# Kernel optimization log

Measured on AMD Instinct MI355X. Metric: run time of the kernel, lower is better.

Reference implementation:

```python
import jax, jax.numpy as jnp
import numpy as np

SEG = 24      # segment_size
NH = 8        # n_heads
THETA = 10000.0


def setup_inputs() -> dict:
    key = jax.random.key(0)
    ks = jax.random.split(key, 6)
    B, T, H, W, D = 8, 96, 32, 32, 64
    in_dim = SEG * D          # 1536
    hid_dim = (SEG // 2) * D  # 768
    n_seg = T // SEG          # 4
    x = jax.random.normal(ks[0], (B, T, H, W, D), dtype=jnp.float32)
    # rotary frequencies: freqs_cis[t, j] = exp(i * t * theta^{-2j/hid_dim})
    inv = 1.0 / (THETA ** (np.arange(0, hid_dim, 2, dtype=np.float32) / hid_dim))
    ang = np.arange(n_seg, dtype=np.float32)[:, None] * inv[None, :]  # (n, hid/2)
    freqs_cos = jnp.asarray(np.cos(ang), dtype=jnp.float32)
    freqs_sin = jnp.asarray(np.sin(ang), dtype=jnp.float32)
    s = 0.02
    Wq = jax.random.normal(ks[1], (in_dim, hid_dim), dtype=jnp.float32) * s
    Wk = jax.random.normal(ks[2], (in_dim, hid_dim), dtype=jnp.float32) * s
    Wv = jax.random.normal(ks[3], (in_dim, hid_dim), dtype=jnp.float32) * s
    Wo = jax.random.normal(ks[4], (hid_dim, in_dim), dtype=jnp.float32) * s
    bo = jnp.zeros((in_dim,), dtype=jnp.float32)
    return {"x": x, "freqs_cos": freqs_cos, "freqs_sin": freqs_sin,
            "Wq": Wq, "Wk": Wk, "Wv": Wv, "Wo": Wo, "bo": bo}


def _rope(q, cos, sin):
    # q: (b, n, hid); pairs (even, odd) rotated by complex multiply
    q2 = q.reshape(*q.shape[:-1], -1, 2)
    qr = q2[..., 0] * cos - q2[..., 1] * sin
    qi = q2[..., 0] * sin + q2[..., 1] * cos
    return jnp.stack([qr, qi], axis=-1).reshape(q.shape)


def reference(x, freqs_cos, freqs_sin, Wq, Wk, Wv, Wo, bo):
    B, T, H, W, D = x.shape
    n = T // SEG
    hid = Wq.shape[1]
    hd = hid // NH
    # (b t h w d) -> ((b h w) n (p d)) ; T divisible by SEG so no padding
    xr = jnp.transpose(x, (0, 2, 3, 1, 4)).reshape(B * H * W, T, D)
    xs = xr.reshape(B * H * W, n, SEG * D)
    q = jnp.einsum('bne,eh->bnh', xs, Wq)
    k = jnp.einsum('bne,eh->bnh', xs, Wk)
    v = jnp.einsum('bne,eh->bnh', xs, Wv)
    cos, sin = freqs_cos[:n][None], freqs_sin[:n][None]  # (1, n, hid/2)
    q = _rope(q, cos, sin)
    k = _rope(k, cos, sin)
    # split heads: b n (h d) -> b h n d
    def heads(t):
        return jnp.transpose(t.reshape(B * H * W, n, NH, hd), (0, 2, 1, 3))
    qh, kh, vh = heads(q), heads(k), heads(v)
    scores = jnp.einsum('bhnd,bhmd->bhnm', qh, kh) / jnp.sqrt(jnp.float32(hd))
    attn = jax.nn.softmax(scores, axis=-1)
    o = jnp.einsum('bhnm,bhmd->bhnd', attn, vh)
    o = jnp.transpose(o, (0, 2, 1, 3)).reshape(B * H * W, n, hid)
    o = jnp.einsum('bnh,he->bne', o, Wo) + bo
    # b n (p d) -> b (n p) d -> (B,T,H,W,D)
    o = o.reshape(B * H * W, T, D)
    o = o.reshape(B, H, W, T, D)
    return jnp.transpose(o, (0, 3, 1, 2, 4))
```

## Files before the change

### kernel.cpp

```cpp
#include <hip/hip_runtime.h>
#include <hip/hip_bf16.h>

using bf16 = __hip_bfloat16;
using short8 = __attribute__((ext_vector_type(8))) short;
using floatx4 = __attribute__((ext_vector_type(4))) float;

#define NSEG 4
#define HID 768
#define INDIM 1536
#define NQKV 2304
#define NHEADS 8
#define HD 96

__device__ inline unsigned short f2b(float v) {
  union { float f; unsigned u; } c; c.f = v;
  unsigned r = c.u + 0x7FFF + ((c.u >> 16) & 1);
  return (unsigned short)(r >> 16);
}

__device__ inline void gload16(const void* g, void* l) {
  __builtin_amdgcn_global_load_lds(
      (const __attribute__((address_space(1))) unsigned int*)g,
      (__attribute__((address_space(3))) unsigned int*)l, 16, 0, 0);
}

#define MEMFENCE asm volatile("" ::: "memory")
#define BARRIER do { MEMFENCE; __builtin_amdgcn_s_barrier(); MEMFENCE; } while (0)

#define PHASE(par, q, LOADB, STAGES, VMW) do {                                 \
    short8 a00 = *(const short8*)(lA + (par)*65536 + (q)*2048);                \
    short8 a01 = *(const short8*)(lA + (par)*65536 + (q)*2048 + 16384);        \
    short8 a10 = *(const short8*)(lA + (par)*65536 + (q)*2048 + 1024);         \
    short8 a11 = *(const short8*)(lA + (par)*65536 + (q)*2048 + 1024 + 16384); \
    if (LOADB) {                                                               \
      _Pragma("unroll")                                                        \
      for (int fn = 0; fn < 4; ++fn) {                                         \
        bfr[fn][0] = *(const short8*)(lB + (par)*65536 + fn*1024);             \
        bfr[fn][1] = *(const short8*)(lB + (par)*65536 + fn*1024 + 16384);     \
      }                                                                        \
    }                                                                          \
    STAGES;                                                                    \
    BARRIER;                                                                   \
    __builtin_amdgcn_s_setprio(1);                                             \
    _Pragma("unroll")                                                          \
    for (int fn = 0; fn < 4; ++fn) {                                           \
      acc[2*(q)][fn]   = __builtin_amdgcn_mfma_f32_16x16x32_bf16(              \
          a00, bfr[fn][0], acc[2*(q)][fn], 0, 0, 0);                           \
      acc[2*(q)][fn]   = __builtin_amdgcn_mfma_f32_16x16x32_bf16(              \
          a01, bfr[fn][1], acc[2*(q)][fn], 0, 0, 0);                           \
      acc[2*(q)+1][fn] = __builtin_amdgcn_mfma_f32_16x16x32_bf16(              \
          a10, bfr[fn][0], acc[2*(q)+1][fn], 0, 0, 0);                         \
      acc[2*(q)+1][fn] = __builtin_amdgcn_mfma_f32_16x16x32_bf16(              \
          a11, bfr[fn][1], acc[2*(q)+1][fn], 0, 0, 0);                         \
    }                                                                          \
    __builtin_amdgcn_s_setprio(0);                                             \
    VMW;                                                                       \
    BARRIER;                                                                   \
  } while (0)

#define VM4 do { asm volatile("s_waitcnt vmcnt(4)" ::: "memory"); } while (0)
#define VM0 do { asm volatile("s_waitcnt vmcnt(0)" ::: "memory"); } while (0)

__global__ __launch_bounds__(256) void transpose_w(
    const float* __restrict__ src, bf16* __restrict__ dst, int K, int C) {
  __shared__ unsigned short tile[32][33];
  const int c0 = blockIdx.x * 32, k0 = blockIdx.y * 32;
  const int tx = threadIdx.x, ty = threadIdx.y;
#pragma unroll
  for (int i = 0; i < 4; ++i)
    tile[ty + 8 * i][tx] = f2b(src[(size_t)(k0 + ty + 8 * i) * C + c0 + tx]);
  __syncthreads();
  unsigned short* d = (unsigned short*)dst;
#pragma unroll
  for (int i = 0; i < 4; ++i)
    d[(size_t)(c0 + ty + 8 * i) * K + k0 + tx] = tile[tx][ty + 8 * i];
}

__global__ __launch_bounds__(256) void convert_x(
    const float* __restrict__ x, bf16* __restrict__ xb) {
  const size_t i = ((size_t)blockIdx.x * 256 + threadIdx.x) * 8;
  float4 a = *(const float4*)(x + i);
  float4 b = *(const float4*)(x + i + 4);
  union { uint4 u; unsigned short s[8]; } r;
  r.s[0] = f2b(a.x); r.s[1] = f2b(a.y); r.s[2] = f2b(a.z); r.s[3] = f2b(a.w);
  r.s[4] = f2b(b.x); r.s[5] = f2b(b.y); r.s[6] = f2b(b.z); r.s[7] = f2b(b.w);
  *(uint4*)(xb + i) = r.u;
}

__global__ __launch_bounds__(512, 2) void gemm_qkv(
    const bf16* __restrict__ xb, const bf16* __restrict__ wT,
    bf16* __restrict__ qkv) {
  __shared__ __align__(16) char lds[131072];
  const int tid = threadIdx.x;
  const int lane = tid & 63, wave = tid >> 6;
  const int wr = wave >> 2, wc = wave & 3;
  const int l15 = lane & 15, quad = lane >> 4;

  const int lt = (blockIdx.x & 7) * 144 + (blockIdx.x >> 3);
  const int n0 = (lt % 9) * 256;
  const int m0 = (lt / 9) * 256;

  const int srow = wave * 16 + (lane >> 2);
  const int dswz = ((lane & 3) * 8) ^ ((lane & 32) >> 1);
  const bf16* asrc[2];
  const bf16* bsrc[2];
#pragma unroll
  for (int h = 0; h < 2; ++h) {
    const int m = m0 + h * 128 + srow;
    const int r = m >> 2, n = m & 3;
    const int b = r >> 10, hw = r & 1023;
    asrc[h] = xb + ((size_t)((b * 96 + n * 24) * 1024 + hw)) * 64 + dswz;
    bsrc[h] = wT + (size_t)(n0 + h * 128 + srow) * INDIM + dswz;
  }
  char* sdst = lds + wave * 1024;

#define STAGE_QA(kt, h) do {                                   \
    char* d_ = sdst + (((kt) & 1) * 65536) + (h) * 8192;       \
    const bf16* s_ = asrc[h] + (size_t)(kt) * 65536;           \
    gload16(s_, d_);                                           \
    gload16(s_ + 32, d_ + 16384);                              \
  } while (0)
#define STAGE_QB(kt, h) do {                                   \
    char* d_ = sdst + 32768 + (((kt) & 1) * 65536) + (h) * 8192; \
    const bf16* s_ = bsrc[h] + (size_t)(kt) * 64;              \
    gload16(s_, d_);                                           \
    gload16(s_ + 32, d_ + 16384);                              \
  } while (0)

  const int lofs = l15 * 64 + ((quad * 16) ^ ((l15 & 8) << 2));
  const char* lA = lds + wr * 8192 + lofs;
  const char* lB = lds + 32768 + wc * 4096 + lofs;

  floatx4 acc[8][4] = {};
  short8 bfr[4][2];

  STAGE_QB(0, 0); STAGE_QB(0, 1); STAGE_QA(0, 0); STAGE_QA(0, 1);
  STAGE_QB(1, 0); STAGE_QB(1, 1);
  VM4;
  BARRIER;

  const int NKT = 24;
  for (int i = 0; i < 12; ++i) {
    const int a = 2 * i;
    PHASE(0, 0, 1, { STAGE_QA(a + 1, 0); }, {});
    PHASE(0, 1, 0, { STAGE_QA(a + 1, 1); }, {});
    PHASE(0, 2, 0, { if (a + 2 < NKT) STAGE_QB(a + 2, 0); }, {});
    PHASE(0, 3, 0, { if (a + 2 < NKT) STAGE_QB(a + 2, 1); },
          { if (a + 2 < NKT) VM4; else VM0; });
    PHASE(1, 0, 1, { if (a + 2 < NKT) STAGE_QA(a + 2, 0); }, {});
    PHASE(1, 1, 0, { if (a + 2 < NKT) STAGE_QA(a + 2, 1); }, {});
    PHASE(1, 2, 0, { if (a + 3 < NKT) STAGE_QB(a + 3, 0); }, {});
    PHASE(1, 3, 0, { if (a + 3 < NKT) STAGE_QB(a + 3, 1); },
          { if (a + 3 < NKT) VM4; else VM0; });
  }
#undef STAGE_QA
#undef STAGE_QB

#pragma unroll
  for (int fm = 0; fm < 8; ++fm)
#pragma unroll
    for (int fn = 0; fn < 4; ++fn)
#pragma unroll
      for (int reg = 0; reg < 4; ++reg) {
        const int row = m0 + wr * 128 + fm * 16 + quad * 4 + reg;
        const int col = n0 + wc * 64 + fn * 16 + l15;
        qkv[(size_t)row * NQKV + col] = __float2bfloat16(acc[fm][fn][reg]);
      }
}

__global__ __launch_bounds__(256) void attn_kernel(
    const bf16* __restrict__ qkv, const float* __restrict__ fcos,
    const float* __restrict__ fsin, bf16* __restrict__ obuf) {
  constexpr int SF_LD = 2312;
  __shared__ float sf[NSEG][SF_LD];
  __shared__ float ssc[NHEADS][NSEG][NSEG];
  __shared__ float sat[NHEADS][NSEG][NSEG];
  const int r = blockIdx.x;
  const int tid = threadIdx.x;
  const bf16* base = qkv + (size_t)r * NSEG * NQKV;

  for (int cid = tid; cid < (NSEG * NQKV) / 8; cid += 256) {
    const int n = cid / (NQKV / 8);
    const int c = (cid % (NQKV / 8)) * 8;
    uint4 u = *(const uint4*)(base + (size_t)n * NQKV + c);
    const bf16* h = reinterpret_cast<const bf16*>(&u);
#pragma unroll
    for (int j = 0; j < 8; ++j) sf[n][c + j] = __bfloat162float(h[j]);
  }
  __syncthreads();

  for (int idx = tid; idx < NSEG * (HID / 2); idx += 256) {
    const int n = idx / (HID / 2), j = idx % (HID / 2);
    const float c = fcos[n * (HID / 2) + j];
    const float s = fsin[n * (HID / 2) + j];
    float q0 = sf[n][2 * j], q1 = sf[n][2 * j + 1];
    sf[n][2 * j] = q0 * c - q1 * s;
    sf[n][2 * j + 1] = q0 * s + q1 * c;
    float k0 = sf[n][HID + 2 * j], k1 = sf[n][HID + 2 * j + 1];
    sf[n][HID + 2 * j] = k0 * c - k1 * s;
    sf[n][HID + 2 * j + 1] = k0 * s + k1 * c;
  }
  __syncthreads();

  if (tid < 128) {
    const int h = tid >> 4, n = (tid >> 2) & 3, m = tid & 3;
    const float* qp = &sf[n][h * HD];
    const float* kp = &sf[m][HID + h * HD];
    float s = 0.f;
#pragma unroll 8
    for (int i = 0; i < HD; ++i) s += qp[i] * kp[i];
    ssc[h][n][m] = s * 0.10206207261596575f;
  }
  __syncthreads();

  if (tid < 32) {
    const int h = tid >> 2, n = tid & 3;
    float mx = ssc[h][n][0];
#pragma unroll
    for (int m = 1; m < 4; ++m) mx = fmaxf(mx, ssc[h][n][m]);
    float e[4], sum = 0.f;
#pragma unroll
    for (int m = 0; m < 4; ++m) { e[m] = __expf(ssc[h][n][m] - mx); sum += e[m]; }
    const float inv = 1.f / sum;
#pragma unroll
    for (int m = 0; m < 4; ++m) sat[h][n][m] = e[m] * inv;
  }
  __syncthreads();

  for (int idx = tid; idx < NSEG * HID; idx += 256) {
    const int n = idx / HID, c = idx % HID, h = c / HD;
    float s = 0.f;
#pragma unroll
    for (int m = 0; m < 4; ++m) s += sat[h][n][m] * sf[m][2 * HID + c];
    obuf[((size_t)r * NSEG + n) * HID + c] = __float2bfloat16(s);
  }
}

__global__ __launch_bounds__(512, 2) void gemm_out(
    const bf16* __restrict__ Ao, const bf16* __restrict__ wT,
    const float* __restrict__ bo, float* __restrict__ out) {
  __shared__ __align__(16) char lds[131072];
  const int tid = threadIdx.x;
  const int lane = tid & 63, wave = tid >> 6;
  const int wr = wave >> 2, wc = wave & 3;
  const int l15 = lane & 15, quad = lane >> 4;

  const int lt = (blockIdx.x & 7) * 96 + (blockIdx.x >> 3);
  const int n0 = (lt % 6) * 256;
  const int m0 = (lt / 6) * 256;

  const int srow = wave * 16 + (lane >> 2);
  const int dswz = ((lane & 3) * 8) ^ ((lane & 32) >> 1);
  const bf16* asrc[2];
  const bf16* bsrc[2];
#pragma unroll
  for (int h = 0; h < 2; ++h) {
    asrc[h] = Ao + (size_t)(m0 + h * 128 + srow) * HID + dswz;
    bsrc[h] = wT + (size_t)(n0 + h * 128 + srow) * HID + dswz;
  }
  char* sdst = lds + wave * 1024;

#define STAGE_OA(kt, h) do {                                   \
    char* d_ = sdst + (((kt) & 1) * 65536) + (h) * 8192;       \
    const bf16* s_ = asrc[h] + (size_t)(kt) * 64;              \
    gload16(s_, d_);                                           \
    gload16(s_ + 32, d_ + 16384);                              \
  } while (0)
#define STAGE_OB(kt, h) do {                                   \
    char* d_ = sdst + 32768 + (((kt) & 1) * 65536) + (h) * 8192; \
    const bf16* s_ = bsrc[h] + (size_t)(kt) * 64;              \
    gload16(s_, d_);                                           \
    gload16(s_ + 32, d_ + 16384);                              \
  } while (0)

  const int lofs = l15 * 64 + ((quad * 16) ^ ((l15 & 8) << 2));
  const char* lA = lds + wr * 8192 + lofs;
  const char* lB = lds + 32768 + wc * 4096 + lofs;

  floatx4 acc[8][4] = {};
  short8 bfr[4][2];

  STAGE_OB(0, 0); STAGE_OB(0, 1); STAGE_OA(0, 0); STAGE_OA(0, 1);
  STAGE_OB(1, 0); STAGE_OB(1, 1);
  VM4;
  BARRIER;

  const int NKT = 12;
  for (int i = 0; i < 6; ++i) {
    const int a = 2 * i;
    PHASE(0, 0, 1, { STAGE_OA(a + 1, 0); }, {});
    PHASE(0, 1, 0, { STAGE_OA(a + 1, 1); }, {});
    PHASE(0, 2, 0, { if (a + 2 < NKT) STAGE_OB(a + 2, 0); }, {});
    PHASE(0, 3, 0, { if (a + 2 < NKT) STAGE_OB(a + 2, 1); },
          { if (a + 2 < NKT) VM4; else VM0; });
    PHASE(1, 0, 1, { if (a + 2 < NKT) STAGE_OA(a + 2, 0); }, {});
    PHASE(1, 1, 0, { if (a + 2 < NKT) STAGE_OA(a + 2, 1); }, {});
    PHASE(1, 2, 0, { if (a + 3 < NKT) STAGE_OB(a + 3, 0); }, {});
    PHASE(1, 3, 0, { if (a + 3 < NKT) STAGE_OB(a + 3, 1); },
          { if (a + 3 < NKT) VM4; else VM0; });
  }
#undef STAGE_OA
#undef STAGE_OB

#pragma unroll
  for (int fm = 0; fm < 8; ++fm)
#pragma unroll
    for (int fn = 0; fn < 4; ++fn)
#pragma unroll
      for (int reg = 0; reg < 4; ++reg) {
        const int row = m0 + wr * 128 + fm * 16 + quad * 4 + reg;
        const int col = n0 + wc * 64 + fn * 16 + l15;
        const float v = acc[fm][fn][reg] + bo[col];
        const int r = row >> 2, n = row & 3;
        const int b = r >> 10, hw = r & 1023;
        const int p = col >> 6, d = col & 63;
        const size_t dst =
            ((size_t)((b * 96 + n * 24 + p) * 1024 + hw)) * 64 + d;
        out[dst] = v;
      }
}

extern "C" void kernel_launch(void* const* d_in, const int* in_sizes, int n_in,
                              void* d_out, int out_size, void* d_ws,
                              size_t ws_size, hipStream_t stream) {
  const float* x = (const float*)d_in[0];
  const float* fcos = (const float*)d_in[1];
  const float* fsin = (const float*)d_in[2];
  const float* Wq = (const float*)d_in[3];
  const float* Wk = (const float*)d_in[4];
  const float* Wv = (const float*)d_in[5];
  const float* Wo = (const float*)d_in[6];
  const float* bo = (const float*)d_in[7];
  float* out = (float*)d_out;

  char* ws = (char*)d_ws;
  bf16* wqkvT = (bf16*)ws;
  bf16* woT = (bf16*)(ws + 7077888);
  bf16* qkv = (bf16*)(ws + 9437184);
  bf16* obuf = (bf16*)(ws + 160432128);
  bf16* xb = (bf16*)d_out;

  dim3 tb(32, 8);
  transpose_w<<<dim3(24, 48), tb, 0, stream>>>(Wq, wqkvT, INDIM, HID);
  transpose_w<<<dim3(24, 48), tb, 0, stream>>>(Wk, wqkvT + (size_t)HID * INDIM, INDIM, HID);
  transpose_w<<<dim3(24, 48), tb, 0, stream>>>(Wv, wqkvT + (size_t)2 * HID * INDIM, INDIM, HID);
  transpose_w<<<dim3(48, 24), tb, 0, stream>>>(Wo, woT, HID, INDIM);

  convert_x<<<24576, 256, 0, stream>>>(x, xb);
  gemm_qkv<<<1152, 512, 0, stream>>>(xb, wqkvT, qkv);
  attn_kernel<<<8192, 256, 0, stream>>>(qkv, fcos, fsin, obuf);
  gemm_out<<<768, 512, 0, stream>>>(obuf, woT, bo, out);
}
```

Measured before the change: 706.5 us.

## Rewrite attention as one wave per row with register-resident shuffle reductions

```diff
diff --git a/kernel.cpp b/kernel.cpp
--- a/kernel.cpp
+++ b/kernel.cpp
@@ -16,6 +16,9 @@
   union { float f; unsigned u; } c; c.f = v;
   unsigned r = c.u + 0x7FFF + ((c.u >> 16) & 1);
   return (unsigned short)(r >> 16);
+}
+__device__ inline float b2f(unsigned short u) {
+  union { unsigned v; float f; } c; c.v = ((unsigned)u) << 16; return c.f;
 }
 
 __device__ inline void gload16(const void* g, void* l) {
@@ -76,6 +79,25 @@
     d[(size_t)(c0 + ty + 8 * i) * K + k0 + tx] = tile[tx][ty + 8 * i];
 }
 
+__global__ __launch_bounds__(256) void transpose_w3(
+    const float* __restrict__ s0, const float* __restrict__ s1,
+    const float* __restrict__ s2, bf16* __restrict__ dst) {
+  __shared__ unsigned short tile[32][33];
+  const float* srcs[3] = {s0, s1, s2};
+  const float* src = srcs[blockIdx.z];
+  bf16* dz = dst + (size_t)blockIdx.z * HID * INDIM;
+  const int c0 = blockIdx.x * 32, k0 = blockIdx.y * 32;
+  const int tx = threadIdx.x, ty = threadIdx.y;
+#pragma unroll
+  for (int i = 0; i < 4; ++i)
+    tile[ty + 8 * i][tx] = f2b(src[(size_t)(k0 + ty + 8 * i) * HID + c0 + tx]);
+  __syncthreads();
+  unsigned short* d = (unsigned short*)dz;
+#pragma unroll
+  for (int i = 0; i < 4; ++i)
+    d[(size_t)(c0 + ty + 8 * i) * INDIM + k0 + tx] = tile[tx][ty + 8 * i];
+}
+
 __global__ __launch_bounds__(256) void convert_x(
     const float* __restrict__ x, bf16* __restrict__ xb) {
   const size_t i = ((size_t)blockIdx.x * 256 + threadIdx.x) * 8;
@@ -171,68 +193,90 @@
 __global__ __launch_bounds__(256) void attn_kernel(
     const bf16* __restrict__ qkv, const float* __restrict__ fcos,
     const float* __restrict__ fsin, bf16* __restrict__ obuf) {
-  constexpr int SF_LD = 2312;
-  __shared__ float sf[NSEG][SF_LD];
-  __shared__ float ssc[NHEADS][NSEG][NSEG];
-  __shared__ float sat[NHEADS][NSEG][NSEG];
-  const int r = blockIdx.x;
-  const int tid = threadIdx.x;
-  const bf16* base = qkv + (size_t)r * NSEG * NQKV;
-
-  for (int cid = tid; cid < (NSEG * NQKV) / 8; cid += 256) {
-    const int n = cid / (NQKV / 8);
-    const int c = (cid % (NQKV / 8)) * 8;
-    uint4 u = *(const uint4*)(base + (size_t)n * NQKV + c);
-    const bf16* h = reinterpret_cast<const bf16*>(&u);
-#pragma unroll
-    for (int j = 0; j < 8; ++j) sf[n][c + j] = __bfloat162float(h[j]);
-  }
-  __syncthreads();
-
-  for (int idx = tid; idx < NSEG * (HID / 2); idx += 256) {
-    const int n = idx / (HID / 2), j = idx % (HID / 2);
-    const float c = fcos[n * (HID / 2) + j];
-    const float s = fsin[n * (HID / 2) + j];
-    float q0 = sf[n][2 * j], q1 = sf[n][2 * j + 1];
-    sf[n][2 * j] = q0 * c - q1 * s;
-    sf[n][2 * j + 1] = q0 * s + q1 * c;
-    float k0 = sf[n][HID + 2 * j], k1 = sf[n][HID + 2 * j + 1];
-    sf[n][HID + 2 * j] = k0 * c - k1 * s;
-    sf[n][HID + 2 * j + 1] = k0 * s + k1 * c;
-  }
-  __syncthreads();
-
-  if (tid < 128) {
-    const int h = tid >> 4, n = (tid >> 2) & 3, m = tid & 3;
-    const float* qp = &sf[n][h * HD];
-    const float* kp = &sf[m][HID + h * HD];
-    float s = 0.f;
-#pragma unroll 8
-    for (int i = 0; i < HD; ++i) s += qp[i] * kp[i];
-    ssc[h][n][m] = s * 0.10206207261596575f;
-  }
-  __syncthreads();
-
-  if (tid < 32) {
-    const int h = tid >> 2, n = tid & 3;
-    float mx = ssc[h][n][0];
-#pragma unroll
-    for (int m = 1; m < 4; ++m) mx = fmaxf(mx, ssc[h][n][m]);
-    float e[4], sum = 0.f;
-#pragma unroll
-    for (int m = 0; m < 4; ++m) { e[m] = __expf(ssc[h][n][m] - mx); sum += e[m]; }
+  const int wave = threadIdx.x >> 6, lane = threadIdx.x & 63;
+  const int r = blockIdx.x * 4 + wave;
+  const int c0 = lane * 12;
+  const int j0 = lane * 6;
+  const bf16* base = qkv + (size_t)r * (NSEG * NQKV) + c0;
+
+  float q[NSEG][12], k[NSEG][12];
+#pragma unroll
+  for (int n = 0; n < NSEG; ++n) {
+    const bf16* row = base + (size_t)n * NQKV;
+    union { uint2 u[3]; unsigned short s[12]; } Q, K;
+#pragma unroll
+    for (int t = 0; t < 3; ++t) {
+      Q.u[t] = *(const uint2*)(row + 4 * t);
+      K.u[t] = *(const uint2*)(row + HID + 4 * t);
+    }
+    const float* cp = fcos + n * (HID / 2) + j0;
+    const float* sp = fsin + n * (HID / 2) + j0;
+#pragma unroll
+    for (int t = 0; t < 6; ++t) {
+      const float cc = cp[t], ss = sp[t];
+      const float a = b2f(Q.s[2 * t]), b = b2f(Q.s[2 * t + 1]);
+      q[n][2 * t] = a * cc - b * ss;
+      q[n][2 * t + 1] = a * ss + b * cc;
+      const float e = b2f(K.s[2 * t]), f = b2f(K.s[2 * t + 1]);
+      k[n][2 * t] = e * cc - f * ss;
+      k[n][2 * t + 1] = e * ss + f * cc;
+    }
+  }
+
+  float P[NSEG][NSEG];
+#pragma unroll
+  for (int n = 0; n < NSEG; ++n)
+#pragma unroll
+    for (int m = 0; m < NSEG; ++m) {
+      float s = 0.f;
+#pragma unroll
+      for (int t = 0; t < 12; ++t) s += q[n][t] * k[m][t];
+      s += __shfl_xor(s, 1, 64);
+      s += __shfl_xor(s, 2, 64);
+      s += __shfl_xor(s, 4, 64);
+      P[n][m] = s * 0.10206207261596575f;
+    }
+#pragma unroll
+  for (int n = 0; n < NSEG; ++n) {
+    const float mx = fmaxf(fmaxf(P[n][0], P[n][1]), fmaxf(P[n][2], P[n][3]));
+    float sum = 0.f;
+#pragma unroll
+    for (int m = 0; m < NSEG; ++m) {
+      P[n][m] = __expf(P[n][m] - mx);
+      sum += P[n][m];
+    }
     const float inv = 1.f / sum;
 #pragma unroll
-    for (int m = 0; m < 4; ++m) sat[h][n][m] = e[m] * inv;
-  }
-  __syncthreads();
-
-  for (int idx = tid; idx < NSEG * HID; idx += 256) {
-    const int n = idx / HID, c = idx % HID, h = c / HD;
-    float s = 0.f;
-#pragma unroll
-    for (int m = 0; m < 4; ++m) s += sat[h][n][m] * sf[m][2 * HID + c];
-    obuf[((size_t)r * NSEG + n) * HID + c] = __float2bfloat16(s);
+    for (int m = 0; m < NSEG; ++m) P[n][m] *= inv;
+  }
+
+  float v[NSEG][12];
+#pragma unroll
+  for (int n = 0; n < NSEG; ++n) {
+    union { uint2 u[3]; unsigned short s[12]; } V;
+#pragma unroll
+    for (int t = 0; t < 3; ++t)
+      V.u[t] = *(const uint2*)(base + (size_t)n * NQKV + 2 * HID + 4 * t);
+#pragma unroll
+    for (int t = 0; t < 12; ++t) v[n][t] = b2f(V.s[t]);
+  }
+  bf16* orow = obuf + (size_t)r * (NSEG * HID) + c0;
+#pragma unroll
+  for (int n = 0; n < NSEG; ++n) {
+    union { uint2 u[3]; unsigned w[6]; } O;
+#pragma unroll
+    for (int t = 0; t < 6; ++t) {
+      float o0 = 0.f, o1 = 0.f;
+#pragma unroll
+      for (int m = 0; m < NSEG; ++m) {
+        o0 += P[n][m] * v[m][2 * t];
+        o1 += P[n][m] * v[m][2 * t + 1];
+      }
+      O.w[t] = (unsigned)f2b(o0) | ((unsigned)f2b(o1) << 16);
+    }
+#pragma unroll
+    for (int t = 0; t < 3; ++t)
+      *(uint2*)(orow + (size_t)n * HID + 4 * t) = O.u[t];
   }
 }
 
@@ -341,13 +385,11 @@
   bf16* xb = (bf16*)d_out;
 
   dim3 tb(32, 8);
-  transpose_w<<<dim3(24, 48), tb, 0, stream>>>(Wq, wqkvT, INDIM, HID);
-  transpose_w<<<dim3(24, 48), tb, 0, stream>>>(Wk, wqkvT + (size_t)HID * INDIM, INDIM, HID);
-  transpose_w<<<dim3(24, 48), tb, 0, stream>>>(Wv, wqkvT + (size_t)2 * HID * INDIM, INDIM, HID);
+  transpose_w3<<<dim3(24, 48, 3), tb, 0, stream>>>(Wq, Wk, Wv, wqkvT);
   transpose_w<<<dim3(48, 24), tb, 0, stream>>>(Wo, woT, HID, INDIM);
 
   convert_x<<<24576, 256, 0, stream>>>(x, xb);
   gemm_qkv<<<1152, 512, 0, stream>>>(xb, wqkvT, qkv);
-  attn_kernel<<<8192, 256, 0, stream>>>(qkv, fcos, fsin, obuf);
+  attn_kernel<<<2048, 256, 0, stream>>>(qkv, fcos, fsin, obuf);
   gemm_out<<<768, 512, 0, stream>>>(obuf, woT, bo, out);
 }
```

New measurement: 684.3 us. 3.1% less time.
